# Optimization experiments

Measured on AMD Instinct MI355X. Metric: run time of the kernel, lower is better.

## Reference

```python
import jax, jax.numpy as jnp
import numpy as np

N, E = 50000, 800000
H, KC, EC, NH = 64, 64, 32, 4   # hidden, key, edge channels, heads
HPH, KPH = H // NH, KC // NH    # per-head value/key dims (16, 16)


def ssp(x):
    # ShiftedSoftplus
    return jax.nn.softplus(x) - jnp.log(2.0).astype(x.dtype)


def grouped_lin(x, w):
    # x: (N, NH, in_per_head), w: (NH, out_per_head, in_per_head)
    # equivalent to Conv1d(kernel=1, groups=NH, bias=False)
    return jnp.einsum('nhi,hoi->nho', x, w)


def lin(x, w, b):
    return x @ w.T + b


def segment_softmax(logits, seg, num_segments):
    # logits: (E, NH), seg: (E,)
    m = jax.ops.segment_max(logits, seg, num_segments=num_segments)
    m = jnp.where(jnp.isfinite(m), m, 0.0)
    e = jnp.exp(logits - m[seg])
    s = jax.ops.segment_sum(e, seg, num_segments=num_segments)
    return e / s[seg]


def setup_inputs() -> dict:
    key = jax.random.key(0)
    ks = jax.random.split(key, 24)
    sc = 0.05
    inp = {
        'x': jax.random.normal(ks[0], (N, H), jnp.float32),
        'edge_index': jax.random.randint(ks[1], (2, E), 0, N, jnp.int64),
        'edge_attr': jax.random.normal(ks[2], (E, EC), jnp.float32),
        # grouped 1x1 convs (block-diagonal linears), no bias
        'k_w': jax.random.normal(ks[3], (NH, KPH, HPH), jnp.float32) * sc,
        'q_w': jax.random.normal(ks[4], (NH, KPH, HPH), jnp.float32) * sc,
        'v_w': jax.random.normal(ks[5], (NH, HPH, HPH), jnp.float32) * sc,
        # weight_k_net: Linear(EC,KPH) -> ssp -> Linear(KPH,KPH)
        'wkn_w1': jax.random.normal(ks[6], (KPH, EC), jnp.float32) * sc,
        'wkn_b1': jnp.zeros((KPH,), jnp.float32),
        'wkn_w2': jax.random.normal(ks[7], (KPH, KPH), jnp.float32) * sc,
        'wkn_b2': jnp.zeros((KPH,), jnp.float32),
        'wkl_w': jax.random.normal(ks[8], (KPH, KPH), jnp.float32) * sc,
        'wkl_b': jnp.zeros((KPH,), jnp.float32),
        # weight_v_net: Linear(EC,HPH) -> ssp -> Linear(HPH,HPH)
        'wvn_w1': jax.random.normal(ks[9], (HPH, EC), jnp.float32) * sc,
        'wvn_b1': jnp.zeros((HPH,), jnp.float32),
        'wvn_w2': jax.random.normal(ks[10], (HPH, HPH), jnp.float32) * sc,
        'wvn_b2': jnp.zeros((HPH,), jnp.float32),
        'wvl_w': jax.random.normal(ks[11], (HPH, HPH), jnp.float32) * sc,
        'wvl_b': jnp.zeros((HPH,), jnp.float32),
        'cen_w': jax.random.normal(ks[12], (H, H), jnp.float32) * sc,
        'cen_b': jnp.zeros((H,), jnp.float32),
        'out_w': jax.random.normal(ks[13], (H, H), jnp.float32) * sc,
        'out_b': jnp.zeros((H,), jnp.float32),
    }
    return inp


def reference(x, edge_index, edge_attr, k_w, q_w, v_w,
              wkn_w1, wkn_b1, wkn_w2, wkn_b2, wkl_w, wkl_b,
              wvn_w1, wvn_b1, wvn_w2, wvn_b2, wvl_w, wvl_b,
              cen_w, cen_b, out_w, out_b):
    n = x.shape[0]
    row, col = edge_index[0], edge_index[1]
    xh = x.reshape(n, NH, HPH)                       # per-head split of channels
    h_keys = grouped_lin(xh, k_w)                    # (N, NH, KPH)
    h_queries = grouped_lin(xh, q_w)                 # (N, NH, KPH)
    h_values = grouped_lin(xh, v_w)                  # (N, NH, HPH)

    W_k = lin(ssp(lin(edge_attr, wkn_w1, wkn_b1)), wkn_w2, wkn_b2)   # (E, KPH)
    keys_j = lin(W_k[:, None, :] * h_keys[col], wkl_w, wkl_b)        # (E, NH, KPH)
    queries_i = h_queries[row]                                       # (E, NH, KPH)
    qk_ij = jnp.sum(queries_i * keys_j, axis=-1)                     # (E, NH)
    alpha = segment_softmax(qk_ij, row, n)                           # (E, NH)

    W_v = lin(ssp(lin(edge_attr, wvn_w1, wvn_b1)), wvn_w2, wvn_b2)   # (E, HPH)
    msg_j = lin(W_v[:, None, :] * h_values[col], wvl_w, wvl_b)       # (E, NH, HPH)
    msg_j = alpha[:, :, None] * msg_j
    aggr = jax.ops.segment_sum(msg_j, row, num_segments=n).reshape(n, H)

    out = lin(x, cen_w, cen_b) + aggr
    return lin(ssp(out), out_w, out_b)
```

## Files before the change

### kernel.cpp

```cpp
#include <hip/hip_runtime.h>
#include <math.h>
#include <stdint.h>

#define NN 50000
#define NE 800000
#define HD 64
#define ECH 32
#define NHEAD 4
#define NBLK 196

__device__ __forceinline__ float ssp_f(float v) {
    return fmaxf(v, 0.0f) + log1pf(__expf(-fabsf(v))) - 0.69314718055994531f;
}

__device__ __forceinline__ uint32_t f2bf_bits(float f) {
    uint32_t u = __float_as_uint(f);
    return (u + 0x7FFFu + ((u >> 16) & 1u)) >> 16;
}
__device__ __forceinline__ float bf2f(uint32_t b) { return __uint_as_float(b << 16); }

__device__ __forceinline__ void unpack8(uint4 p, float* o) {
    o[0] = bf2f(p.x & 0xffffu); o[1] = bf2f(p.x >> 16);
    o[2] = bf2f(p.y & 0xffffu); o[3] = bf2f(p.y >> 16);
    o[4] = bf2f(p.z & 0xffffu); o[5] = bf2f(p.z >> 16);
    o[6] = bf2f(p.w & 0xffffu); o[7] = bf2f(p.w >> 16);
}
__device__ __forceinline__ uint4 pack8(const float* s) {
    uint4 r;
    r.x = f2bf_bits(s[0]) | (f2bf_bits(s[1]) << 16);
    r.y = f2bf_bits(s[2]) | (f2bf_bits(s[3]) << 16);
    r.z = f2bf_bits(s[4]) | (f2bf_bits(s[5]) << 16);
    r.w = f2bf_bits(s[6]) | (f2bf_bits(s[7]) << 16);
    return r;
}

__global__ __launch_bounds__(256) void node_transform_kernel(
    const float* __restrict__ x,
    const float* __restrict__ k_w, const float* __restrict__ q_w, const float* __restrict__ v_w,
    const float* __restrict__ wkl_w, const float* __restrict__ wkl_b,
    uint16_t* __restrict__ qt, float* __restrict__ qb,
    uint16_t* __restrict__ hk, uint16_t* __restrict__ hv)
{
    __shared__ float skw[NHEAD * 256], sqw[NHEAD * 256], svw[NHEAD * 256];
    __shared__ float s_kl[256], s_klb[16];
    for (int i = threadIdx.x; i < NHEAD * 256; i += 256) {
        skw[i] = k_w[i]; sqw[i] = q_w[i]; svw[i] = v_w[i];
    }
    if (threadIdx.x < 256) s_kl[threadIdx.x] = wkl_w[threadIdx.x];
    if (threadIdx.x < 16) s_klb[threadIdx.x] = wkl_b[threadIdx.x];
    __syncthreads();
    int n = blockIdx.x * 256 + threadIdx.x;
    if (n >= NN) return;
    const float* xn = x + (size_t)n * HD;
    float qbv[NHEAD];
    for (int h = 0; h < NHEAD; ++h) {
        float xr[16];
        {
            const float4* xp = (const float4*)(xn + h * 16);
            #pragma unroll
            for (int j = 0; j < 4; ++j) *(float4*)&xr[4 * j] = xp[j];
        }
        float rq[16], rk[16], rv[16];
        for (int o = 0; o < 16; ++o) {
            const float* wq = sqw + h * 256 + o * 16;
            const float* wk = skw + h * 256 + o * 16;
            const float* wv = svw + h * 256 + o * 16;
            float sq = 0.f, sk = 0.f, sv = 0.f;
            #pragma unroll
            for (int i = 0; i < 16; ++i) {
                sq += xr[i] * wq[i];
                sk += xr[i] * wk[i];
                sv += xr[i] * wv[i];
            }
            rq[o] = sq; rk[o] = sk; rv[o] = sv;
        }
        float rqt[16];
        float qbh = 0.f;
        for (int i = 0; i < 16; ++i) {
            float s = 0.f;
            #pragma unroll
            for (int o = 0; o < 16; ++o) s += rq[o] * s_kl[o * 16 + i];
            rqt[i] = s;
        }
        #pragma unroll
        for (int o = 0; o < 16; ++o) qbh += rq[o] * s_klb[o];
        qbv[h] = qbh;

        uint4* oq = (uint4*)(qt + (size_t)n * HD + h * 16);
        uint4* ok = (uint4*)(hk + (size_t)n * HD + h * 16);
        uint4* ov = (uint4*)(hv + (size_t)n * HD + h * 16);
        oq[0] = pack8(rqt); oq[1] = pack8(rqt + 8);
        ok[0] = pack8(rk);  ok[1] = pack8(rk + 8);
        ov[0] = pack8(rv);  ov[1] = pack8(rv + 8);
    }
    *(float4*)(qb + (size_t)n * NHEAD) = *(float4*)&qbv[0];
}

__global__ __launch_bounds__(256) void count_kernel(
    const int* __restrict__ ei, int* __restrict__ counts)
{
    int e = blockIdx.x * 256 + threadIdx.x;
    if (e >= NE) return;
    atomicAdd(counts + ei[e], 1);
}

__global__ __launch_bounds__(256) void scan_bsum_kernel(
    const int* __restrict__ counts, int* __restrict__ bsum)
{
    __shared__ int sd[256];
    int i = blockIdx.x * 256 + threadIdx.x;
    sd[threadIdx.x] = (i < NN) ? counts[i] : 0;
    __syncthreads();
    for (int s = 128; s > 0; s >>= 1) {
        if (threadIdx.x < (unsigned)s) sd[threadIdx.x] += sd[threadIdx.x + s];
        __syncthreads();
    }
    if (threadIdx.x == 0) bsum[blockIdx.x] = sd[0];
}

__global__ __launch_bounds__(256) void scan_top_kernel(int* __restrict__ bsum)
{
    __shared__ int tmp[256];
    int v = (threadIdx.x < NBLK) ? bsum[threadIdx.x] : 0;
    tmp[threadIdx.x] = v;
    __syncthreads();
    for (int d = 1; d < 256; d <<= 1) {
        int t = (threadIdx.x >= (unsigned)d) ? tmp[threadIdx.x - d] : 0;
        __syncthreads();
        tmp[threadIdx.x] += t;
        __syncthreads();
    }
    if (threadIdx.x < NBLK) bsum[threadIdx.x] = tmp[threadIdx.x] - v;
}

__global__ __launch_bounds__(256) void scan_final_kernel(
    const int* __restrict__ counts, const int* __restrict__ bsum,
    int* __restrict__ offsets, int* __restrict__ cursor)
{
    __shared__ int tmp[256];
    int i = blockIdx.x * 256 + threadIdx.x;
    int v = (i < NN) ? counts[i] : 0;
    tmp[threadIdx.x] = v;
    __syncthreads();
    for (int d = 1; d < 256; d <<= 1) {
        int t = (threadIdx.x >= (unsigned)d) ? tmp[threadIdx.x - d] : 0;
        __syncthreads();
        tmp[threadIdx.x] += t;
        __syncthreads();
    }
    int excl = tmp[threadIdx.x] - v + bsum[blockIdx.x];
    if (i < NN) { offsets[i] = excl; cursor[i] = excl; }
}

__global__ __launch_bounds__(256) void edge_compute_kernel(
    const int* __restrict__ ei,
    const float* __restrict__ ea,
    const float* __restrict__ wkn_w1, const float* __restrict__ wkn_b1,
    const float* __restrict__ wkn_w2, const float* __restrict__ wkn_b2,
    const float* __restrict__ wvn_w1, const float* __restrict__ wvn_b1,
    const float* __restrict__ wvn_w2, const float* __restrict__ wvn_b2,
    const uint16_t* __restrict__ qt, const float* __restrict__ qb,
    const uint16_t* __restrict__ hk, const uint16_t* __restrict__ hv,
    int* __restrict__ cursor,
    uint16_t* __restrict__ payload, float* __restrict__ wfac)
{
    __shared__ float s_kn1[512], s_vn1[512];
    __shared__ float s_kn2[256], s_vn2[256];
    __shared__ float s_knb1[16], s_knb2[16], s_vnb1[16], s_vnb2[16];
    for (int i = threadIdx.x; i < 512; i += 256) { s_kn1[i] = wkn_w1[i]; s_vn1[i] = wvn_w1[i]; }
    if (threadIdx.x < 256) { s_kn2[threadIdx.x] = wkn_w2[threadIdx.x]; s_vn2[threadIdx.x] = wvn_w2[threadIdx.x]; }
    if (threadIdx.x < 16) {
        s_knb1[threadIdx.x] = wkn_b1[threadIdx.x]; s_knb2[threadIdx.x] = wkn_b2[threadIdx.x];
        s_vnb1[threadIdx.x] = wvn_b1[threadIdx.x]; s_vnb2[threadIdx.x] = wvn_b2[threadIdx.x];
    }
    __syncthreads();
    int e = blockIdx.x * 256 + threadIdx.x;
    if (e >= NE) return;

    int row = ei[e];
    int col = ei[NE + e];

    float eav[32];
    {
        const float4* p = (const float4*)(ea + (size_t)e * ECH);
        #pragma unroll
        for (int i = 0; i < 8; ++i) *(float4*)&eav[4 * i] = p[i];
    }

    float h1k[16], h1v[16];
    for (int o = 0; o < 16; ++o) {
        float sk = s_knb1[o], sv = s_vnb1[o];
        #pragma unroll
        for (int i = 0; i < 32; ++i) {
            sk += eav[i] * s_kn1[o * 32 + i];
            sv += eav[i] * s_vn1[o * 32 + i];
        }
        h1k[o] = ssp_f(sk);
        h1v[o] = ssp_f(sv);
    }
    float Wk[16], Wv[16];
    for (int o = 0; o < 16; ++o) {
        float sk = s_knb2[o], sv = s_vnb2[o];
        #pragma unroll
        for (int i = 0; i < 16; ++i) {
            sk += h1k[i] * s_kn2[o * 16 + i];
            sv += h1v[i] * s_vn2[o * 16 + i];
        }
        Wk[o] = sk; Wv[o] = sv;
    }

    int pos = atomicAdd(cursor + row, 1);

    float4 qbv = *(const float4*)(qb + (size_t)row * NHEAD);
    const float qbarr[4] = {qbv.x, qbv.y, qbv.z, qbv.w};
    const uint4* qtb = (const uint4*)(qt + (size_t)row * HD);
    const uint4* kb  = (const uint4*)(hk + (size_t)col * HD);
    const uint4* vb  = (const uint4*)(hv + (size_t)col * HD);
    uint4* pd = (uint4*)(payload + (size_t)pos * HD);
    float wf[NHEAD];

    #pragma unroll
    for (int h = 0; h < NHEAD; ++h) {
        float qr[16], kc[16], vc[16];
        unpack8(qtb[2 * h], qr); unpack8(qtb[2 * h + 1], qr + 8);
        unpack8(kb[2 * h], kc);  unpack8(kb[2 * h + 1], kc + 8);
        unpack8(vb[2 * h], vc);  unpack8(vb[2 * h + 1], vc + 8);
        float qk = qbarr[h];
        #pragma unroll
        for (int i = 0; i < 16; ++i) qk += qr[i] * Wk[i] * kc[i];
        float w = __expf(qk);
        wf[h] = w;
        float o0[8], o1[8];
        #pragma unroll
        for (int i = 0; i < 8; ++i) o0[i] = w * Wv[i] * vc[i];
        #pragma unroll
        for (int i = 0; i < 8; ++i) o1[i] = w * Wv[8 + i] * vc[8 + i];
        pd[2 * h]     = pack8(o0);
        pd[2 * h + 1] = pack8(o1);
    }
    *(float4*)(wfac + (size_t)pos * NHEAD) = *(float4*)&wf[0];
}

__global__ __launch_bounds__(256) void gather_finalize_kernel(
    const float* __restrict__ x,
    const uint16_t* __restrict__ payload, const float* __restrict__ wfac,
    const int* __restrict__ offsets, const int* __restrict__ counts,
    const float* __restrict__ wvl_w, const float* __restrict__ wvl_b,
    const float* __restrict__ cen_w, const float* __restrict__ cen_b,
    const float* __restrict__ out_w, const float* __restrict__ out_b,
    float* __restrict__ out)
{
    __shared__ float s_cw[4096], s_ow[4096];
    __shared__ float s_wvl[256], s_vlb[16];
    __shared__ float s_m[4][64], s_x[4][64], s_t[4][64];
    for (int idx = threadIdx.x; idx < 4096; idx += 256) {
        int o = idx & 63, i = idx >> 6;
        s_cw[i * 64 + o] = cen_w[o * 64 + i];
        s_ow[i * 64 + o] = out_w[o * 64 + i];
    }
    if (threadIdx.x < 256) s_wvl[threadIdx.x] = wvl_w[threadIdx.x];
    if (threadIdx.x < 16) s_vlb[threadIdx.x] = wvl_b[threadIdx.x];
    __syncthreads();

    int l = threadIdx.x >> 6;
    int L = threadIdx.x & 63;
    int q = L & 15, g = L >> 4;
    int head4 = q >> 2;

    for (int t = 0; t < 4; ++t) {
        int n = blockIdx.x * 16 + l * 4 + t;
        bool valid = n < NN;
        int st = 0, deg = 0;
        if (valid) { st = offsets[n]; deg = counts[n]; }
        float u0 = 0.f, u1 = 0.f, u2 = 0.f, u3 = 0.f, ds = 0.f;
        const uint16_t* pp = payload + (size_t)st * HD + 4 * q;
        const float* wp = wfac + (size_t)st * NHEAD + head4;
        int iters = (deg + 3) >> 2;
        for (int i = 0; i < iters; ++i) {
            int e = i * 4 + g;
            if (e < deg) {
                uint2 pv = *(const uint2*)(pp + (size_t)e * HD);
                u0 += bf2f(pv.x & 0xffffu); u1 += bf2f(pv.x >> 16);
                u2 += bf2f(pv.y & 0xffffu); u3 += bf2f(pv.y >> 16);
                ds += wp[(size_t)e * NHEAD];
            }
        }
        u0 += __shfl_xor(u0, 16); u1 += __shfl_xor(u1, 16);
        u2 += __shfl_xor(u2, 16); u3 += __shfl_xor(u3, 16);
        ds += __shfl_xor(ds, 16);
        u0 += __shfl_xor(u0, 32); u1 += __shfl_xor(u1, 32);
        u2 += __shfl_xor(u2, 32); u3 += __shfl_xor(u3, 32);
        ds += __shfl_xor(ds, 32);

        float m0 = 0.f, m1 = 0.f, m2 = 0.f, m3 = 0.f;
        if (deg > 0) {
            float inv = 1.f / ds;
            m0 = u0 * inv; m1 = u1 * inv; m2 = u2 * inv; m3 = u3 * inv;
        }
        float msel = (g == 0) ? m0 : (g == 1) ? m1 : (g == 2) ? m2 : m3;
        s_m[l][4 * q + g] = msel;
        s_x[l][L] = valid ? x[(size_t)n * HD + L] : 0.f;

        int c = L, h = c >> 4;
        float aggr = 0.f;
        if (deg > 0) {
            int o = c & 15;
            float s = s_vlb[o];
            #pragma unroll
            for (int i = 0; i < 16; ++i) s += s_m[l][h * 16 + i] * s_wvl[o * 16 + i];
            aggr = s;
        }
        float sc = cen_b[c];
        #pragma unroll 8
        for (int i = 0; i < 64; ++i) sc += s_x[l][i] * s_cw[i * 64 + c];
        sc += aggr;
        s_t[l][c] = ssp_f(sc);
        float so = out_b[c];
        #pragma unroll 8
        for (int i = 0; i < 64; ++i) so += s_t[l][i] * s_ow[i * 64 + c];
        if (valid) out[(size_t)n * HD + c] = so;
    }
}

extern "C" void kernel_launch(void* const* d_in, const int* in_sizes, int n_in,
                              void* d_out, int out_size, void* d_ws, size_t ws_size,
                              hipStream_t stream)
{
    const float* x      = (const float*)d_in[0];
    const int*   ei     = (const int*)d_in[1];
    const float* ea     = (const float*)d_in[2];
    const float* k_w    = (const float*)d_in[3];
    const float* q_w    = (const float*)d_in[4];
    const float* v_w    = (const float*)d_in[5];
    const float* wkn_w1 = (const float*)d_in[6];
    const float* wkn_b1 = (const float*)d_in[7];
    const float* wkn_w2 = (const float*)d_in[8];
    const float* wkn_b2 = (const float*)d_in[9];
    const float* wkl_w  = (const float*)d_in[10];
    const float* wkl_b  = (const float*)d_in[11];
    const float* wvn_w1 = (const float*)d_in[12];
    const float* wvn_b1 = (const float*)d_in[13];
    const float* wvn_w2 = (const float*)d_in[14];
    const float* wvn_b2 = (const float*)d_in[15];
    const float* wvl_w  = (const float*)d_in[16];
    const float* wvl_b  = (const float*)d_in[17];
    const float* cen_w  = (const float*)d_in[18];
    const float* cen_b  = (const float*)d_in[19];
    const float* out_w  = (const float*)d_in[20];
    const float* out_b  = (const float*)d_in[21];
    float* out = (float*)d_out;

    float* qb    = (float*)d_ws;
    float* wfac  = qb + (size_t)NN * NHEAD;
    uint16_t* qt = (uint16_t*)(wfac + (size_t)NE * NHEAD);
    uint16_t* hk = qt + (size_t)NN * HD;
    uint16_t* hv = hk + (size_t)NN * HD;
    uint16_t* payload = hv + (size_t)NN * HD;
    int* counts  = (int*)(payload + (size_t)NE * HD);
    int* bsum    = counts + NN;
    int* offsets = bsum + 256;
    int* cursor  = offsets + NN;

    hipMemsetAsync(counts, 0, (size_t)NN * sizeof(int), stream);
    node_transform_kernel<<<NBLK, 256, 0, stream>>>(
        x, k_w, q_w, v_w, wkl_w, wkl_b, qt, qb, hk, hv);
    count_kernel<<<(NE + 255) / 256, 256, 0, stream>>>(ei, counts);
    scan_bsum_kernel<<<NBLK, 256, 0, stream>>>(counts, bsum);
    scan_top_kernel<<<1, 256, 0, stream>>>(bsum);
    scan_final_kernel<<<NBLK, 256, 0, stream>>>(counts, bsum, offsets, cursor);
    edge_compute_kernel<<<(NE + 255) / 256, 256, 0, stream>>>(
        ei, ea, wkn_w1, wkn_b1, wkn_w2, wkn_b2,
        wvn_w1, wvn_b1, wvn_w2, wvn_b2,
        qt, qb, hk, hv, cursor, payload, wfac);
    gather_finalize_kernel<<<(NN + 15) / 16, 256, 0, stream>>>(
        x, payload, wfac, offsets, counts,
        wvl_w, wvl_b, cen_w, cen_b, out_w, out_b, out);
}
```

Baseline: 556.2 us.

## Compute edge MLPs with bf16 MFMA and process edges in row-sorted order

Adds a separate scatter kernel that sorts edges by destination row into an edge list plus a (row,col) array. The edge kernel then works in sorted order, so payload and weight-factor writes become contiguous and row-indexed q loads become more local. The two-layer edge MLPs now run on MFMA 16x16x32 bf16 instructions, with shared-memory transposes between layers, replacing the scalar FMA loops. In exchange it adds a kernel launch, extra workspace, and bf16 rounding of edge_attr and the hidden activations, and edge_attr reads become indirect gathers.

New measurement: 566.4 us. No clear change (+1.8%).

```diff
diff --git a/kernel.cpp b/kernel.cpp
--- a/kernel.cpp
+++ b/kernel.cpp
@@ -9,10 +9,14 @@
 #define NHEAD 4
 #define NBLK 196
 
+static_assert(NE % 256 == 0, "edge kernel assumes full blocks");
+
+typedef __attribute__((ext_vector_type(8))) short bf8;
+typedef __attribute__((ext_vector_type(4))) float f32x4;
+
 __device__ __forceinline__ float ssp_f(float v) {
     return fmaxf(v, 0.0f) + log1pf(__expf(-fabsf(v))) - 0.69314718055994531f;
 }
-
 __device__ __forceinline__ uint32_t f2bf_bits(float f) {
     uint32_t u = __float_as_uint(f);
     return (u + 0x7FFFu + ((u >> 16) & 1u)) >> 16;
@@ -25,12 +29,26 @@
     o[4] = bf2f(p.z & 0xffffu); o[5] = bf2f(p.z >> 16);
     o[6] = bf2f(p.w & 0xffffu); o[7] = bf2f(p.w >> 16);
 }
-__device__ __forceinline__ uint4 pack8(const float* s) {
+__device__ __forceinline__ uint4 pack8u(const float* s) {
     uint4 r;
     r.x = f2bf_bits(s[0]) | (f2bf_bits(s[1]) << 16);
     r.y = f2bf_bits(s[2]) | (f2bf_bits(s[3]) << 16);
     r.z = f2bf_bits(s[4]) | (f2bf_bits(s[5]) << 16);
     r.w = f2bf_bits(s[6]) | (f2bf_bits(s[7]) << 16);
+    return r;
+}
+__device__ __forceinline__ bf8 pack_bf8(float4 a, float4 b) {
+    bf8 r;
+    r[0] = (short)f2bf_bits(a.x); r[1] = (short)f2bf_bits(a.y);
+    r[2] = (short)f2bf_bits(a.z); r[3] = (short)f2bf_bits(a.w);
+    r[4] = (short)f2bf_bits(b.x); r[5] = (short)f2bf_bits(b.y);
+    r[6] = (short)f2bf_bits(b.z); r[7] = (short)f2bf_bits(b.w);
+    return r;
+}
+__device__ __forceinline__ bf8 zero_bf8() {
+    bf8 r;
+    #pragma unroll
+    for (int i = 0; i < 8; ++i) r[i] = 0;
     return r;
 }
 
@@ -89,9 +107,9 @@
         uint4* oq = (uint4*)(qt + (size_t)n * HD + h * 16);
         uint4* ok = (uint4*)(hk + (size_t)n * HD + h * 16);
         uint4* ov = (uint4*)(hv + (size_t)n * HD + h * 16);
-        oq[0] = pack8(rqt); oq[1] = pack8(rqt + 8);
-        ok[0] = pack8(rk);  ok[1] = pack8(rk + 8);
-        ov[0] = pack8(rv);  ov[1] = pack8(rv + 8);
+        oq[0] = pack8u(rqt); oq[1] = pack8u(rqt + 8);
+        ok[0] = pack8u(rk);  ok[1] = pack8u(rk + 8);
+        ov[0] = pack8u(rv);  ov[1] = pack8u(rv + 8);
     }
     *(float4*)(qb + (size_t)n * NHEAD) = *(float4*)&qbv[0];
 }
@@ -152,8 +170,21 @@
     if (i < NN) { offsets[i] = excl; cursor[i] = excl; }
 }
 
+__global__ __launch_bounds__(256) void scatter_kernel(
+    const int* __restrict__ ei, int* __restrict__ cursor,
+    int* __restrict__ elist, int2* __restrict__ rc)
+{
+    int e = blockIdx.x * 256 + threadIdx.x;
+    if (e >= NE) return;
+    int r = ei[e];
+    int c = ei[NE + e];
+    int pos = atomicAdd(cursor + r, 1);
+    elist[pos] = e;
+    rc[pos] = make_int2(r, c);
+}
+
 __global__ __launch_bounds__(256) void edge_compute_kernel(
-    const int* __restrict__ ei,
+    const int* __restrict__ elist, const int2* __restrict__ rc,
     const float* __restrict__ ea,
     const float* __restrict__ wkn_w1, const float* __restrict__ wkn_b1,
     const float* __restrict__ wkn_w2, const float* __restrict__ wkn_b2,
@@ -161,62 +192,109 @@
     const float* __restrict__ wvn_w2, const float* __restrict__ wvn_b2,
     const uint16_t* __restrict__ qt, const float* __restrict__ qb,
     const uint16_t* __restrict__ hk, const uint16_t* __restrict__ hv,
-    int* __restrict__ cursor,
     uint16_t* __restrict__ payload, float* __restrict__ wfac)
 {
-    __shared__ float s_kn1[512], s_vn1[512];
-    __shared__ float s_kn2[256], s_vn2[256];
-    __shared__ float s_knb1[16], s_knb2[16], s_vnb1[16], s_vnb2[16];
-    for (int i = threadIdx.x; i < 512; i += 256) { s_kn1[i] = wkn_w1[i]; s_vn1[i] = wvn_w1[i]; }
-    if (threadIdx.x < 256) { s_kn2[threadIdx.x] = wkn_w2[threadIdx.x]; s_vn2[threadIdx.x] = wvn_w2[threadIdx.x]; }
-    if (threadIdx.x < 16) {
-        s_knb1[threadIdx.x] = wkn_b1[threadIdx.x]; s_knb2[threadIdx.x] = wkn_b2[threadIdx.x];
-        s_vnb1[threadIdx.x] = wvn_b1[threadIdx.x]; s_vnb2[threadIdx.x] = wvn_b2[threadIdx.x];
-    }
-    __syncthreads();
-    int e = blockIdx.x * 256 + threadIdx.x;
-    if (e >= NE) return;
-
-    int row = ei[e];
-    int col = ei[NE + e];
-
-    float eav[32];
+    __shared__ uint16_t s_tr1[4][64][24];
+    __shared__ uint16_t s_trk[4][64][24];
+    __shared__ uint16_t s_trv[4][64][24];
+
+    const int w = threadIdx.x >> 6;
+    const int L = threadIdx.x & 63;
+    const int m = L & 15;
+    const int g = L >> 4;
+    const int ebase = blockIdx.x * 256 + w * 64;
+
+    bf8 eaf[4];
+    #pragma unroll
+    for (int t = 0; t < 4; ++t) {
+        int eid = elist[ebase + 16 * t + m];
+        const float* er = ea + (size_t)eid * ECH + 8 * g;
+        eaf[t] = pack_bf8(*(const float4*)er, *(const float4*)(er + 4));
+    }
+    bf8 w1kf, w1vf, w2kf, w2vf;
     {
-        const float4* p = (const float4*)(ea + (size_t)e * ECH);
-        #pragma unroll
-        for (int i = 0; i < 8; ++i) *(float4*)&eav[4 * i] = p[i];
-    }
-
-    float h1k[16], h1v[16];
-    for (int o = 0; o < 16; ++o) {
-        float sk = s_knb1[o], sv = s_vnb1[o];
-        #pragma unroll
-        for (int i = 0; i < 32; ++i) {
-            sk += eav[i] * s_kn1[o * 32 + i];
-            sv += eav[i] * s_vn1[o * 32 + i];
-        }
-        h1k[o] = ssp_f(sk);
-        h1v[o] = ssp_f(sv);
-    }
+        const float* p = wkn_w1 + m * 32 + 8 * g;
+        w1kf = pack_bf8(*(const float4*)p, *(const float4*)(p + 4));
+        p = wvn_w1 + m * 32 + 8 * g;
+        w1vf = pack_bf8(*(const float4*)p, *(const float4*)(p + 4));
+        if (g < 2) {
+            p = wkn_w2 + m * 16 + 8 * g;
+            w2kf = pack_bf8(*(const float4*)p, *(const float4*)(p + 4));
+            p = wvn_w2 + m * 16 + 8 * g;
+            w2vf = pack_bf8(*(const float4*)p, *(const float4*)(p + 4));
+        } else {
+            w2kf = zero_bf8(); w2vf = zero_bf8();
+        }
+    }
+    float4 b1k = *(const float4*)(wkn_b1 + 4 * g);
+    float4 b1v = *(const float4*)(wvn_b1 + 4 * g);
+    float4 b2k = *(const float4*)(wkn_b2 + 4 * g);
+    float4 b2v = *(const float4*)(wvn_b2 + 4 * g);
+
+    #pragma unroll
+    for (int t = 0; t < 4; ++t) {
+        f32x4 acc = {b1k.x, b1k.y, b1k.z, b1k.w};
+        acc = __builtin_amdgcn_mfma_f32_16x16x32_bf16(w1kf, eaf[t], acc, 0, 0, 0);
+        uint2 pk;
+        pk.x = f2bf_bits(ssp_f(acc[0])) | (f2bf_bits(ssp_f(acc[1])) << 16);
+        pk.y = f2bf_bits(ssp_f(acc[2])) | (f2bf_bits(ssp_f(acc[3])) << 16);
+        *(uint2*)&s_tr1[w][16 * t + m][4 * g] = pk;
+    }
+    __syncthreads();
+    bf8 l1k[4];
+    #pragma unroll
+    for (int t = 0; t < 4; ++t)
+        l1k[t] = (g < 2) ? *(const bf8*)&s_tr1[w][16 * t + m][8 * g] : zero_bf8();
+    __syncthreads();
+    #pragma unroll
+    for (int t = 0; t < 4; ++t) {
+        f32x4 acc = {b1v.x, b1v.y, b1v.z, b1v.w};
+        acc = __builtin_amdgcn_mfma_f32_16x16x32_bf16(w1vf, eaf[t], acc, 0, 0, 0);
+        uint2 pk;
+        pk.x = f2bf_bits(ssp_f(acc[0])) | (f2bf_bits(ssp_f(acc[1])) << 16);
+        pk.y = f2bf_bits(ssp_f(acc[2])) | (f2bf_bits(ssp_f(acc[3])) << 16);
+        *(uint2*)&s_tr1[w][16 * t + m][4 * g] = pk;
+    }
+    __syncthreads();
+    bf8 l1v[4];
+    #pragma unroll
+    for (int t = 0; t < 4; ++t)
+        l1v[t] = (g < 2) ? *(const bf8*)&s_tr1[w][16 * t + m][8 * g] : zero_bf8();
+
+    #pragma unroll
+    for (int t = 0; t < 4; ++t) {
+        f32x4 acc = {b2k.x, b2k.y, b2k.z, b2k.w};
+        acc = __builtin_amdgcn_mfma_f32_16x16x32_bf16(w2kf, l1k[t], acc, 0, 0, 0);
+        uint2 pk;
+        pk.x = f2bf_bits(acc[0]) | (f2bf_bits(acc[1]) << 16);
+        pk.y = f2bf_bits(acc[2]) | (f2bf_bits(acc[3]) << 16);
+        *(uint2*)&s_trk[w][16 * t + m][4 * g] = pk;
+
+        f32x4 accv = {b2v.x, b2v.y, b2v.z, b2v.w};
+        accv = __builtin_amdgcn_mfma_f32_16x16x32_bf16(w2vf, l1v[t], accv, 0, 0, 0);
+        uint2 pv;
+        pv.x = f2bf_bits(accv[0]) | (f2bf_bits(accv[1]) << 16);
+        pv.y = f2bf_bits(accv[2]) | (f2bf_bits(accv[3]) << 16);
+        *(uint2*)&s_trv[w][16 * t + m][4 * g] = pv;
+    }
+    __syncthreads();
+
+    const int E = ebase + L;
+    int2 rcv = rc[E];
+    const int row = rcv.x, col = rcv.y;
+
     float Wk[16], Wv[16];
-    for (int o = 0; o < 16; ++o) {
-        float sk = s_knb2[o], sv = s_vnb2[o];
-        #pragma unroll
-        for (int i = 0; i < 16; ++i) {
-            sk += h1k[i] * s_kn2[o * 16 + i];
-            sv += h1v[i] * s_vn2[o * 16 + i];
-        }
-        Wk[o] = sk; Wv[o] = sv;
-    }
-
-    int pos = atomicAdd(cursor + row, 1);
+    unpack8(*(const uint4*)&s_trk[w][L][0], Wk);
+    unpack8(*(const uint4*)&s_trk[w][L][8], Wk + 8);
+    unpack8(*(const uint4*)&s_trv[w][L][0], Wv);
+    unpack8(*(const uint4*)&s_trv[w][L][8], Wv + 8);
 
     float4 qbv = *(const float4*)(qb + (size_t)row * NHEAD);
     const float qbarr[4] = {qbv.x, qbv.y, qbv.z, qbv.w};
     const uint4* qtb = (const uint4*)(qt + (size_t)row * HD);
     const uint4* kb  = (const uint4*)(hk + (size_t)col * HD);
     const uint4* vb  = (const uint4*)(hv + (size_t)col * HD);
-    uint4* pd = (uint4*)(payload + (size_t)pos * HD);
+    uint4* pd = (uint4*)(payload + (size_t)E * HD);
     float wf[NHEAD];
 
     #pragma unroll
@@ -228,17 +306,17 @@
         float qk = qbarr[h];
         #pragma unroll
         for (int i = 0; i < 16; ++i) qk += qr[i] * Wk[i] * kc[i];
-        float w = __expf(qk);
-        wf[h] = w;
+        float wgt = __expf(qk);
+        wf[h] = wgt;
         float o0[8], o1[8];
         #pragma unroll
-        for (int i = 0; i < 8; ++i) o0[i] = w * Wv[i] * vc[i];
+        for (int i = 0; i < 8; ++i) o0[i] = wgt * Wv[i] * vc[i];
         #pragma unroll
-        for (int i = 0; i < 8; ++i) o1[i] = w * Wv[8 + i] * vc[8 + i];
-        pd[2 * h]     = pack8(o0);
-        pd[2 * h + 1] = pack8(o1);
-    }
-    *(float4*)(wfac + (size_t)pos * NHEAD) = *(float4*)&wf[0];
+        for (int i = 0; i < 8; ++i) o1[i] = wgt * Wv[8 + i] * vc[8 + i];
+        pd[2 * h]     = pack8u(o0);
+        pd[2 * h + 1] = pack8u(o1);
+    }
+    *(float4*)(wfac + (size_t)E * NHEAD) = *(float4*)&wf[0];
 }
 
 __global__ __launch_bounds__(256) void gather_finalize_kernel(
@@ -356,7 +434,9 @@
     uint16_t* hk = qt + (size_t)NN * HD;
     uint16_t* hv = hk + (size_t)NN * HD;
     uint16_t* payload = hv + (size_t)NN * HD;
-    int* counts  = (int*)(payload + (size_t)NE * HD);
+    int2* rc     = (int2*)(payload + (size_t)NE * HD);
+    int* elist   = (int*)(rc + (size_t)NE);
+    int* counts  = elist + NE;
     int* bsum    = counts + NN;
     int* offsets = bsum + 256;
     int* cursor  = offsets + NN;
@@ -368,10 +448,11 @@
     scan_bsum_kernel<<<NBLK, 256, 0, stream>>>(counts, bsum);
     scan_top_kernel<<<1, 256, 0, stream>>>(bsum);
     scan_final_kernel<<<NBLK, 256, 0, stream>>>(counts, bsum, offsets, cursor);
-    edge_compute_kernel<<<(NE + 255) / 256, 256, 0, stream>>>(
-        ei, ea, wkn_w1, wkn_b1, wkn_w2, wkn_b2,
+    scatter_kernel<<<(NE + 255) / 256, 256, 0, stream>>>(ei, cursor, elist, rc);
+    edge_compute_kernel<<<NE / 256, 256, 0, stream>>>(
+        elist, rc, ea, wkn_w1, wkn_b1, wkn_w2, wkn_b2,
         wvn_w1, wvn_b1, wvn_w2, wvn_b2,
-        qt, qb, hk, hv, cursor, payload, wfac);
+        qt, qb, hk, hv, payload, wfac);
     gather_finalize_kernel<<<(NN + 15) / 16, 256, 0, stream>>>(
         x, payload, wfac, offsets, counts,
         wvl_w, wvl_b, cen_w, cen_b, out_w, out_b, out);
```
